# Performance work log

Hardware: AMD Instinct MI355X
Metric: run time of the kernel (lower is better)

The kernel has to match this reference:

```python
import jax, jax.numpy as jnp
import numpy as np
from jax import lax

B, X, H, W, C = 4, 32, 8, 128, 32  # batch, frames, height, width, channels (dim)


def setup_inputs() -> dict:
    key = jax.random.key(0)
    k1, k2, k3, k4, k5, k6 = jax.random.split(key, 6)
    return {
        "storage": jax.random.normal(k1, (B, X, H, W, C), jnp.float32),
        "target": jax.random.normal(k2, (B, 1, H, W, C), jnp.float32),
        # Conv3d(dim, 2*dim, kernel=(3,1,1), padding=(1,0,0)) weight/bias
        "w_cross": jax.random.normal(k3, (2 * C, C, 3, 1, 1), jnp.float32) * 0.05,
        "b_cross": jax.random.normal(k4, (2 * C,), jnp.float32) * 0.05,
        # Conv2d(dim, dim, kernel=1) weight (stored as [out, in]) / bias
        "w_q": jax.random.normal(k5, (C, C), jnp.float32) * 0.1,
        "b_q": jax.random.normal(k6, (C,), jnp.float32) * 0.1,
    }


def reference(storage, target, w_cross, b_cross, w_q, b_q):
    # storage [B,X,H,W,C] -> transpose(4,1).transpose(4,2) -> [B,C,X,W,H]
    s = jnp.transpose(storage, (0, 4, 1, 3, 2))
    # target [B,1,H,W,C] -> transpose(4,2) -> [B,1,C,W,H] -> squeeze(1) -> [B,C,W,H]
    t = jnp.transpose(target, (0, 1, 4, 3, 2))[:, 0]

    # Conv3d over the X (depth) axis, kernel (3,1,1), padding (1,0,0)
    out = lax.conv_general_dilated(
        s, w_cross, window_strides=(1, 1, 1),
        padding=((1, 1), (0, 0), (0, 0)),
        dimension_numbers=("NCDHW", "OIDHW", "NCDHW"),
    ) + b_cross[None, :, None, None, None]          # [B,2C,X,W,H]
    s_v, s_k = jnp.split(out, 2, axis=1)            # each [B,C,X,W,H]

    # 1x1 Conv2d query projection
    t_q = jnp.einsum("oc,bcwh->bowh", w_q, t) + b_q[None, :, None, None]  # [B,C,W,H]
    # unsqueeze(1).transpose(2,1).repeat over X -> [B,C,X,W,H]
    t_q = jnp.broadcast_to(t_q[:, :, None], (B, C, X, W, H))

    # Faithful torch .view on contiguous [B,C,X,W,H]: row-major reshape mixes C into last dim
    t_q = t_q.reshape(B, X * W, C * H)
    s_v = s_v.reshape(B, X * W, C * H)
    s_k = jnp.swapaxes(s_k.reshape(B, X * W, C * H), 1, 2)  # [B, C*H, X*W]

    kq = jax.nn.softmax(jnp.einsum("bnc,bcm->bnm", t_q, s_k), axis=-1)  # [B, XW, XW]
    final = jnp.einsum("bnm,bmc->bnc", kq, s_v)                          # [B, XW, C*H]
    return final.reshape(B, X, H, W, C)
```

## Files before the change

kernel.cpp:

```cpp
#include <hip/hip_runtime.h>

typedef unsigned short u16;
typedef unsigned int u32;
typedef __attribute__((ext_vector_type(8))) short s16x8;
typedef __attribute__((ext_vector_type(4))) float f32x4;

#define WS_A      0u
#define WS_B      8388608u
#define WS_C      16777216u
#define WS_LP     25452544u
#define WS_NEEDED 25485312u

__device__ __forceinline__ u16 f2bf(float f){
  u32 u = __float_as_uint(f);
  return (u16)((u + 0x7fffu + ((u >> 16) & 1u)) >> 16);
}

__global__ __launch_bounds__(256) void zero_out_kernel(float* __restrict__ out){
  int t = blockIdx.x * 256 + threadIdx.x;
  ((float4*)out)[t] = make_float4(0.f, 0.f, 0.f, 0.f);
}

__global__ __launch_bounds__(256, 4) void conv_kernel(const float* __restrict__ storage,
    const float* __restrict__ w_cross, const float* __restrict__ b_cross,
    u16* __restrict__ Kb, u16* __restrict__ Vb){
  int o_idx = (blockIdx.x & 7) * 128 + (blockIdx.x >> 3);
  int og2 = o_idx & 1;
  int wc  = (o_idx >> 1) & 3;
  int x   = (o_idx >> 3) & 31;
  int b   = o_idx >> 8;
  int tid = threadIdx.x;
  int w4 = tid >> 6;
  int oh = w4 >> 1, mh = w4 & 1;
  int lane = tid & 63, l15 = lane & 15, quad = lane >> 4;

  s16x8 Ahi[3], Alo[3];
  {
    int o = og2*32 + oh*16 + l15;
    const float4* wp = (const float4*)(w_cross + o*96 + quad*24);
    float w24[24];
    #pragma unroll
    for (int i = 0; i < 6; ++i){
      float4 v = wp[i];
      w24[i*4+0] = v.x; w24[i*4+1] = v.y; w24[i*4+2] = v.z; w24[i*4+3] = v.w;
    }
    #pragma unroll
    for (int dx = 0; dx < 3; ++dx){
      #pragma unroll
      for (int e = 0; e < 8; ++e){
        float wv = w24[e*3 + dx];
        u32 u = __float_as_uint(wv);
        float r = wv - __uint_as_float(u & 0xffff0000u);
        Ahi[dx][e] = (short)(u >> 16);
        Alo[dx][e] = (short)(__float_as_uint(r) >> 16);
      }
    }
  }

  f32x4 acc[8];
  {
    float4 bv = *(const float4*)(b_cross + og2*32 + oh*16 + quad*4);
    #pragma unroll
    for (int mt = 0; mt < 8; ++mt) acc[mt] = (f32x4){bv.x, bv.y, bv.z, bv.w};
  }

  #pragma unroll
  for (int dx = 0; dx < 3; ++dx){
    int xx = x + dx - 1;
    if (xx < 0 || xx > 31) continue;
    const float* pb = storage +
        ((((size_t)b*32 + xx)*8 + (l15 & 7))*128 + wc*32 + mh*16 + (l15 >> 3))*32 + quad*8;
    #pragma unroll
    for (int g = 0; g < 2; ++g){
      float4 va[4], vb4[4];
      #pragma unroll
      for (int k = 0; k < 4; ++k){
        va[k]  = *(const float4*)(pb + (g*4 + k)*64);
        vb4[k] = *(const float4*)(pb + (g*4 + k)*64 + 4);
      }
      #pragma unroll
      for (int k = 0; k < 4; ++k){
        int mt = g*4 + k;
        float v[8] = {va[k].x, va[k].y, va[k].z, va[k].w,
                      vb4[k].x, vb4[k].y, vb4[k].z, vb4[k].w};
        s16x8 bhi, blo;
        #pragma unroll
        for (int e = 0; e < 8; ++e){
          u32 u = __float_as_uint(v[e]);
          float r = v[e] - __uint_as_float(u & 0xffff0000u);
          bhi[e] = (short)(u >> 16);
          blo[e] = (short)(__float_as_uint(r) >> 16);
        }
        acc[mt] = __builtin_amdgcn_mfma_f32_16x16x32_bf16(Ahi[dx], bhi, acc[mt], 0, 0, 0);
        acc[mt] = __builtin_amdgcn_mfma_f32_16x16x32_bf16(Ahi[dx], blo, acc[mt], 0, 0, 0);
        acc[mt] = __builtin_amdgcn_mfma_f32_16x16x32_bf16(Alo[dx], bhi, acc[mt], 0, 0, 0);
      }
    }
  }

  __shared__ u16 st[32 * 264];
  #pragma unroll
  for (int mt = 0; mt < 8; ++mt){
    #pragma unroll
    for (int r = 0; r < 4; ++r)
      st[(oh*16 + quad*4 + r)*264 + mh*128 + mt*16 + l15] = f2bf(acc[mt][r]);
  }
  __syncthreads();
  int o_loc = tid >> 3, part = tid & 7;
  size_t base = ((size_t)b*4096 + (size_t)o_loc*128 + (size_t)x*4 + wc)*256 + part*8;
  u16* dst = (og2 == 0 ? Vb : Kb) + base;
  const u16* src = &st[o_loc*264 + part*8];
  #pragma unroll
  for (int i = 0; i < 4; ++i)
    *(uint4*)(dst + i*64) = *(const uint4*)(src + i*64);
}

__global__ __launch_bounds__(256, 2) void flash_kernel(const float* __restrict__ target,
    const float* __restrict__ w_q, const float* __restrict__ b_q,
    const u16* __restrict__ Kb, const u16* __restrict__ Vb,
    float* __restrict__ Opart, float* __restrict__ lpart){
  int kq = blockIdx.x & 15, rb = (blockIdx.x >> 4) & 7, b = blockIdx.x >> 7;
  int tid = threadIdx.x;
  int w = tid >> 6, lane = tid & 63, l15 = lane & 15, quad = lane >> 4;

  __shared__ alignas(16) u16 Vts[256 * 64];
  __shared__ alignas(16) u16 Ps[16 * 64];
  __shared__ float lsumW[64];

  u16* stgQ = Vts;
  {
    int wl = tid & 31, h = tid >> 5;
    #pragma unroll
    for (int wcq = 0; wcq < 4; ++wcq){
      float in[32];
      const float4* p = (const float4*)(target + (((size_t)b*8 + h)*128 + wcq*32 + wl)*32);
      #pragma unroll
      for (int q = 0; q < 8; ++q){
        float4 v = p[q];
        in[q*4+0] = v.x; in[q*4+1] = v.y; in[q*4+2] = v.z; in[q*4+3] = v.w;
      }
      #pragma unroll
      for (int cql = 0; cql < 4; ++cql){
        int cq = rb*4 + cql;
        float acc = b_q[cq];
        #pragma unroll
        for (int c = 0; c < 32; ++c) acc = fmaf(in[c], w_q[cq*32 + c], acc);
        stgQ[(cql*4 + wcq)*264 + wl*8 + h] = f2bf(acc);
      }
    }
  }
  __syncthreads();

  s16x8 qa[8];
  {
    const u16* qp = stgQ + l15*264 + quad*8;
    #pragma unroll
    for (int ks = 0; ks < 8; ++ks) qa[ks] = *(const s16x8*)(qp + ks*32);
  }
  __syncthreads();

  int jl4 = tid & 15, mseg = tid >> 4;
  const u16* kbase = Kb + ((size_t)(b*4096 + kq*256 + w*16 + l15))*256 + quad*8;
  const u16* vbase = Vb + ((size_t)(b*4096 + kq*256 + jl4*4))*256 + mseg*16;

  s16x8 kr[8];
  #pragma unroll
  for (int ks = 0; ks < 8; ++ks) kr[ks] = *(const s16x8*)(kbase + ks*32);
  u32 kv[4][8];
  #pragma unroll
  for (int kk = 0; kk < 4; ++kk){
    uint4 a = *(const uint4*)(vbase + kk*256);
    uint4 b2 = *(const uint4*)(vbase + kk*256 + 8);
    kv[kk][0]=a.x; kv[kk][1]=a.y; kv[kk][2]=a.z; kv[kk][3]=a.w;
    kv[kk][4]=b2.x; kv[kk][5]=b2.y; kv[kk][6]=b2.z; kv[kk][7]=b2.w;
  }

  float lacc[4] = {0.f, 0.f, 0.f, 0.f};
  f32x4 oc[4];
  #pragma unroll
  for (int mt = 0; mt < 4; ++mt) oc[mt] = (f32x4){0.f,0.f,0.f,0.f};

  #pragma unroll
  for (int it = 0; it < 4; ++it){
    if (it > 0) __syncthreads();

    #pragma unroll
    for (int i = 0; i < 16; ++i){
      int d = i >> 1;
      u32 e0, e1, e2, e3;
      if (i & 1){ e0 = kv[0][d] >> 16;     e1 = kv[1][d] >> 16;
                  e2 = kv[2][d] >> 16;     e3 = kv[3][d] >> 16; }
      else      { e0 = kv[0][d] & 0xffffu; e1 = kv[1][d] & 0xffffu;
                  e2 = kv[2][d] & 0xffffu; e3 = kv[3][d] & 0xffffu; }
      int m = mseg*16 + i;
      int col = (((jl4 >> 1) ^ (m & 7)) << 3) + ((jl4 & 1) << 2);
      *(uint2*)&Vts[m*64 + col] = make_uint2(e0 | (e1 << 16), e2 | (e3 << 16));
    }

    f32x4 s0 = {0.f,0.f,0.f,0.f}, s1 = {0.f,0.f,0.f,0.f};
    #pragma unroll
    for (int ks = 0; ks < 8; ks += 2){
      s0 = __builtin_amdgcn_mfma_f32_16x16x32_bf16(qa[ks],   kr[ks],   s0, 0, 0, 0);
      s1 = __builtin_amdgcn_mfma_f32_16x16x32_bf16(qa[ks+1], kr[ks+1], s1, 0, 0, 0);
    }
    int b8k = w*2 + (l15 >> 3);
    #pragma unroll
    for (int reg = 0; reg < 4; ++reg){
      float sv = fminf(s0[reg] + s1[reg], 80.f);
      float p = __expf(sv);
      int row = quad*4 + reg;
      Ps[row*64 + ((b8k ^ (row & 7)) << 3) + (l15 & 7)] = f2bf(p);
      lacc[reg] += p;
    }

    if (it < 3){
      const u16* vp = vbase + (it+1)*16384;
      #pragma unroll
      for (int kk = 0; kk < 4; ++kk){
        uint4 a = *(const uint4*)(vp + kk*256);
        uint4 b2 = *(const uint4*)(vp + kk*256 + 8);
        kv[kk][0]=a.x; kv[kk][1]=a.y; kv[kk][2]=a.z; kv[kk][3]=a.w;
        kv[kk][4]=b2.x; kv[kk][5]=b2.y; kv[kk][6]=b2.z; kv[kk][7]=b2.w;
      }
    }
    __syncthreads();

    if (it < 3){
      const u16* kp = kbase + (it+1)*16384;
      #pragma unroll
      for (int ks = 0; ks < 8; ++ks) kr[ks] = *(const s16x8*)(kp + ks*32);
    }
    #pragma unroll
    for (int ks2 = 0; ks2 < 2; ++ks2){
      int b8 = ks2*4 + quad;
      s16x8 pb = *(const s16x8*)&Ps[l15*64 + ((b8 ^ (l15 & 7)) << 3)];
      #pragma unroll
      for (int mt = 0; mt < 4; ++mt){
        int mrow = (w*4 + mt)*16 + l15;
        s16x8 af = *(const s16x8*)&Vts[mrow*64 + ((b8 ^ (mrow & 7)) << 3)];
        oc[mt] = __builtin_amdgcn_mfma_f32_16x16x32_bf16(af, pb, oc[mt], 0, 0, 0);
      }
    }
  }

  #pragma unroll
  for (int reg = 0; reg < 4; ++reg){
    float t = lacc[reg];
    t += __shfl_xor(t, 1); t += __shfl_xor(t, 2);
    t += __shfl_xor(t, 4); t += __shfl_xor(t, 8);
    lacc[reg] = t;
  }
  if (l15 == 0){
    #pragma unroll
    for (int reg = 0; reg < 4; ++reg) lsumW[w*16 + quad*4 + reg] = lacc[reg];
  }
  __syncthreads();
  if (tid < 16)
    lpart[(b*16 + kq)*128 + rb*16 + tid] =
        lsumW[tid] + lsumW[16 + tid] + lsumW[32 + tid] + lsumW[48 + tid];
  {
    float* dst = Opart + ((size_t)((b*16 + kq)*128 + rb*16 + l15))*256 + w*64 + quad*4;
    #pragma unroll
    for (int mt = 0; mt < 4; ++mt)
      *(float4*)(dst + mt*16) = make_float4(oc[mt][0], oc[mt][1], oc[mt][2], oc[mt][3]);
  }
}

__global__ __launch_bounds__(256) void combine_kernel(const float* __restrict__ lpart,
    const float* __restrict__ Opart, float* __restrict__ out){
  int r = blockIdx.x & 127, b = blockIdx.x >> 7;
  int m = threadIdx.x;
  float L = 0.f, o = 0.f;
  #pragma unroll
  for (int kq = 0; kq < 16; ++kq){
    L += lpart[(b*16 + kq)*128 + r];
    o += Opart[((size_t)((b*16 + kq)*128 + r))*256 + m];
  }
  o /= L;
  int cq = r >> 2, whi = r & 3;
  size_t obase = ((size_t)b*32 + cq) * 32768;
  #pragma unroll
  for (int hh = 0; hh < 8; ++hh){
    #pragma unroll
    for (int wt = 0; wt < 4; ++wt){
      out[obase + hh*4096 + wt*1024 + whi*256 + m] = o;
    }
  }
}

extern "C" void kernel_launch(void* const* d_in, const int* in_sizes, int n_in,
                              void* d_out, int out_size, void* d_ws, size_t ws_size,
                              hipStream_t stream){
  const float* storage = (const float*)d_in[0];
  const float* target  = (const float*)d_in[1];
  const float* w_cross = (const float*)d_in[2];
  const float* b_cross = (const float*)d_in[3];
  const float* w_q     = (const float*)d_in[4];
  const float* b_q     = (const float*)d_in[5];
  float* out = (float*)d_out;

  if (ws_size < (size_t)WS_NEEDED){
    zero_out_kernel<<<dim3(4096), dim3(256), 0, stream>>>(out);
    return;
  }

  char* ws = (char*)d_ws;
  float* Opart = (float*)(ws + WS_A);
  u16*   Kb    = (u16*)(ws + WS_B);
  u16*   Vb    = (u16*)(ws + WS_C);
  float* lpart = (float*)(ws + WS_LP);

  conv_kernel    <<<dim3(1024), dim3(256), 0, stream>>>(storage, w_cross, b_cross, Kb, Vb);
  flash_kernel   <<<dim3(512),  dim3(256), 0, stream>>>(target, w_q, b_q, Kb, Vb, Opart, lpart);
  combine_kernel <<<dim3(512),  dim3(256), 0, stream>>>(lpart, Opart, out);
}
```

Baseline: 139.7 us.

## Stage conv input tiles in LDS and share across both K/V output halves

The conv kernel now uses 512-thread blocks that compute all 64 output channels (V and K) per block. Previously two blocks each reloaded and re-split the same input. Each input frame slice is loaded once, split into bf16 hi/lo in LDS with an XOR swizzle, and double-buffered across the three temporal taps, overlapping the next stage's load with MFMA consumption. This halves global reads and hi/lo conversion work. The cost is 64KB of LDS per block, which limits occupancy, plus extra barriers.

New measurement: 122.0 us. 1.14x faster.

```diff
diff --git a/kernel.cpp b/kernel.cpp
--- a/kernel.cpp
+++ b/kernel.cpp
@@ -21,22 +21,27 @@
   ((float4*)out)[t] = make_float4(0.f, 0.f, 0.f, 0.f);
 }
 
-__global__ __launch_bounds__(256, 4) void conv_kernel(const float* __restrict__ storage,
+__global__ __launch_bounds__(512, 4) void conv_kernel(const float* __restrict__ storage,
     const float* __restrict__ w_cross, const float* __restrict__ b_cross,
     u16* __restrict__ Kb, u16* __restrict__ Vb){
-  int o_idx = (blockIdx.x & 7) * 128 + (blockIdx.x >> 3);
-  int og2 = o_idx & 1;
-  int wc  = (o_idx >> 1) & 3;
-  int x   = (o_idx >> 3) & 31;
-  int b   = o_idx >> 8;
+  __shared__ alignas(16) char smem[65536];
+  u16* Hp0 = (u16*)smem;
+  u16* Lp0 = (u16*)(smem + 16384);
+  u16* Hp1 = (u16*)(smem + 32768);
+  u16* Lp1 = (u16*)(smem + 49152);
+
+  int o_idx = (blockIdx.x & 7) * 64 + (blockIdx.x >> 3);
+  int wc = o_idx & 3;
+  int x  = (o_idx >> 2) & 31;
+  int b  = o_idx >> 7;
   int tid = threadIdx.x;
-  int w4 = tid >> 6;
-  int oh = w4 >> 1, mh = w4 & 1;
+  int w8 = tid >> 6;
+  int oh = w8 >> 1, mh = w8 & 1;
   int lane = tid & 63, l15 = lane & 15, quad = lane >> 4;
 
   s16x8 Ahi[3], Alo[3];
   {
-    int o = og2*32 + oh*16 + l15;
+    int o = oh*16 + l15;
     const float4* wp = (const float4*)(w_cross + o*96 + quad*24);
     float w24[24];
     #pragma unroll
@@ -59,46 +64,69 @@
 
   f32x4 acc[8];
   {
-    float4 bv = *(const float4*)(b_cross + og2*32 + oh*16 + quad*4);
+    float4 bv = *(const float4*)(b_cross + oh*16 + quad*4);
     #pragma unroll
     for (int mt = 0; mt < 8; ++mt) acc[mt] = (f32x4){bv.x, bv.y, bv.z, bv.w};
   }
 
-  #pragma unroll
-  for (int dx = 0; dx < 3; ++dx){
+  auto STAGE = [&](int dx, u16* H, u16* L){
     int xx = x + dx - 1;
-    if (xx < 0 || xx > 31) continue;
-    const float* pb = storage +
-        ((((size_t)b*32 + xx)*8 + (l15 & 7))*128 + wc*32 + mh*16 + (l15 >> 3))*32 + quad*8;
-    #pragma unroll
-    for (int g = 0; g < 2; ++g){
-      float4 va[4], vb4[4];
-      #pragma unroll
-      for (int k = 0; k < 4; ++k){
-        va[k]  = *(const float4*)(pb + (g*4 + k)*64);
-        vb4[k] = *(const float4*)(pb + (g*4 + k)*64 + 4);
-      }
-      #pragma unroll
-      for (int k = 0; k < 4; ++k){
-        int mt = g*4 + k;
-        float v[8] = {va[k].x, va[k].y, va[k].z, va[k].w,
-                      vb4[k].x, vb4[k].y, vb4[k].z, vb4[k].w};
-        s16x8 bhi, blo;
-        #pragma unroll
-        for (int e = 0; e < 8; ++e){
-          u32 u = __float_as_uint(v[e]);
-          float r = v[e] - __uint_as_float(u & 0xffff0000u);
-          bhi[e] = (short)(u >> 16);
-          blo[e] = (short)(__float_as_uint(r) >> 16);
-        }
-        acc[mt] = __builtin_amdgcn_mfma_f32_16x16x32_bf16(Ahi[dx], bhi, acc[mt], 0, 0, 0);
-        acc[mt] = __builtin_amdgcn_mfma_f32_16x16x32_bf16(Ahi[dx], blo, acc[mt], 0, 0, 0);
-        acc[mt] = __builtin_amdgcn_mfma_f32_16x16x32_bf16(Alo[dx], bhi, acc[mt], 0, 0, 0);
-      }
-    }
-  }
-
-  __shared__ u16 st[32 * 264];
+    const float* src = storage + (size_t)(b*32 + xx)*32768;
+    #pragma unroll
+    for (int r = 0; r < 4; ++r){
+      int e = r*2048 + tid*4;
+      int h = e >> 10, w = (e >> 5) & 31, c = e & 31;
+      float4 v = *(const float4*)(src + h*4096 + (wc*32 + w)*32 + c);
+      int idx = (h*32 + w)*32 + (((c >> 3) ^ (h & 3)) << 3) + (c & 7);
+      float f[4] = {v.x, v.y, v.z, v.w};
+      ushort4 hv, lv;
+      u16* hp = (u16*)&hv; u16* lp = (u16*)&lv;
+      #pragma unroll
+      for (int k2 = 0; k2 < 4; ++k2){
+        u32 u = __float_as_uint(f[k2]);
+        float rr = f[k2] - __uint_as_float(u & 0xffff0000u);
+        hp[k2] = (u16)(u >> 16);
+        lp[k2] = (u16)(__float_as_uint(rr) >> 16);
+      }
+      *(ushort4*)&H[idx] = hv;
+      *(ushort4*)&L[idx] = lv;
+    }
+  };
+
+  auto CONSUME = [&](s16x8 ah, s16x8 al, const u16* H, const u16* L){
+    int h = l15 & 7;
+    int cb = quad ^ (h & 3);
+    #pragma unroll
+    for (int mt = 0; mt < 8; ++mt){
+      int wr = mh*16 + mt*2 + (l15 >> 3);
+      int idx = (h*32 + wr)*32 + cb*8;
+      s16x8 bhi = *(const s16x8*)&H[idx];
+      s16x8 blo = *(const s16x8*)&L[idx];
+      acc[mt] = __builtin_amdgcn_mfma_f32_16x16x32_bf16(ah, bhi, acc[mt], 0, 0, 0);
+      acc[mt] = __builtin_amdgcn_mfma_f32_16x16x32_bf16(ah, blo, acc[mt], 0, 0, 0);
+      acc[mt] = __builtin_amdgcn_mfma_f32_16x16x32_bf16(al, bhi, acc[mt], 0, 0, 0);
+    }
+  };
+
+  bool has0 = (x > 0), has2 = (x < 31);
+  if (has0) STAGE(0, Hp0, Lp0); else STAGE(1, Hp1, Lp1);
+  __syncthreads();
+  if (has0){
+    STAGE(1, Hp1, Lp1);
+    CONSUME(Ahi[0], Alo[0], Hp0, Lp0);
+    __syncthreads();
+  }
+  {
+    if (has2) STAGE(2, Hp0, Lp0);
+    CONSUME(Ahi[1], Alo[1], Hp1, Lp1);
+    __syncthreads();
+  }
+  if (has2){
+    CONSUME(Ahi[2], Alo[2], Hp0, Lp0);
+    __syncthreads();
+  }
+
+  u16* st = (u16*)smem;
   #pragma unroll
   for (int mt = 0; mt < 8; ++mt){
     #pragma unroll
@@ -107,12 +135,12 @@
   }
   __syncthreads();
   int o_loc = tid >> 3, part = tid & 7;
-  size_t base = ((size_t)b*4096 + (size_t)o_loc*128 + (size_t)x*4 + wc)*256 + part*8;
-  u16* dst = (og2 == 0 ? Vb : Kb) + base;
-  const u16* src = &st[o_loc*264 + part*8];
+  size_t base = ((size_t)b*4096 + (size_t)(o_loc & 31)*128 + (size_t)x*4 + wc)*256 + part*8;
+  u16* dst = (o_loc < 32 ? Vb : Kb) + base;
+  const u16* srcp = &st[o_loc*264 + part*8];
   #pragma unroll
   for (int i = 0; i < 4; ++i)
-    *(uint4*)(dst + i*64) = *(const uint4*)(src + i*64);
+    *(uint4*)(dst + i*64) = *(const uint4*)(srcp + i*64);
 }
 
 __global__ __launch_bounds__(256, 2) void flash_kernel(const float* __restrict__ target,
@@ -310,7 +338,7 @@
   u16*   Vb    = (u16*)(ws + WS_C);
   float* lpart = (float*)(ws + WS_LP);
 
-  conv_kernel    <<<dim3(1024), dim3(256), 0, stream>>>(storage, w_cross, b_cross, Kb, Vb);
-  flash_kernel   <<<dim3(512),  dim3(256), 0, stream>>>(target, w_q, b_q, Kb, Vb, Opart, lpart);
-  combine_kernel <<<dim3(512),  dim3(256), 0, stream>>>(lpart, Opart, out);
-}
+  conv_kernel    <<<dim3(512), dim3(512), 0, stream>>>(storage, w_cross, b_cross, Kb, Vb);
+  flash_kernel   <<<dim3(512), dim3(256), 0, stream>>>(target, w_q, b_q, Kb, Vb, Opart, lpart);
+  combine_kernel <<<dim3(512), dim3(256), 0, stream>>>(lpart, Opart, out);
+}
```
